# Optimization experiments

Hardware: AMD Instinct MI355X
Metric: run time of the kernel (lower is better)

Reference implementation:

```python
import jax, jax.numpy as jnp
import numpy as np

P = 920   # spatial positions per frame (hard-coded in source)
FRAMES = 5
H = 8     # num_heads
C = 256   # dim


def setup_inputs() -> dict:
    key = jax.random.key(0)
    ks = jax.random.split(key, 6)
    B = 4
    s = 0.02
    return {
        "x": jax.random.normal(ks[0], (P, B * FRAMES, C), dtype=jnp.float32),
        "W_qkv": jax.random.normal(ks[1], (3 * C, C), dtype=jnp.float32) * s,
        "W_pq": jax.random.normal(ks[2], (C, C), dtype=jnp.float32) * s,
        "W_pkv": jax.random.normal(ks[3], (2 * C, C), dtype=jnp.float32) * s,
        "W_proj": jax.random.normal(ks[4], (C, C), dtype=jnp.float32) * s,
        "b_proj": jnp.zeros((C,), dtype=jnp.float32),
    }


def reference(x, W_qkv, W_pq, W_pkv, W_proj, b_proj):
    d = C // H
    scale = d ** -0.5
    N = FRAMES * P

    # (P, B*F, C) -> (B*F, P, C) -> (B, F*P, C)
    xb = jnp.transpose(x, (1, 0, 2)).reshape(-1, N, C)
    B = xb.shape[0]

    # Stage 1: space attention (note: heads are NOT split here, per original code)
    qkv = xb @ W_qkv.T                      # (B, N, 3C)
    q_, k_, v_ = jnp.split(qkv, 3, axis=-1)
    q_dot_k = jnp.einsum('bqc,bnc->bqn', q_, k_)        # (B, N, N)
    q_dot_k = q_dot_k.reshape(B, N, FRAMES, P)          # b q f n
    space_attn = jax.nn.softmax(scale * q_dot_k, axis=-1)
    v_f = v_.reshape(B, FRAMES, P, C)                   # b f n d
    x1 = jnp.einsum('bqfn,bfnd->bqfd', space_attn, v_f)  # (B, N, F, C)

    # Diagonal extraction: each spatial position attends to its own frame
    xg = x1.reshape(B, FRAMES, P, FRAMES, C)            # b g n f d
    x_diag = jnp.diagonal(xg, axis1=1, axis2=3)         # (B, P, C, F)
    x_diag = jnp.transpose(x_diag, (0, 3, 1, 2)).reshape(B, N, C)  # b (f n) d

    # Stage 2: trajectory attention over frames, with heads
    q2 = x_diag @ W_pq.T                                # (B, N, C)
    kv2 = x1 @ W_pkv.T                                  # (B, N, F, 2C)
    k2, v2 = jnp.split(kv2, 2, axis=-1)
    q2 = q2.reshape(B, N, H, d).transpose(0, 2, 1, 3) * scale      # b h s d
    k2 = k2.reshape(B, N, FRAMES, H, d).transpose(0, 3, 1, 2, 4)   # b h s f d
    v2 = v2.reshape(B, N, FRAMES, H, d).transpose(0, 3, 1, 2, 4)
    attn = jax.nn.softmax(jnp.einsum('bhsd,bhsfd->bhsf', q2, k2), axis=-1)
    x2 = jnp.einsum('bhsf,bhsfd->bhsd', attn, v2)       # (B, H, N, d)
    x2 = x2.transpose(0, 2, 1, 3).reshape(B, N, C)

    out = x2 @ W_proj.T + b_proj                        # (B, N, C)
    out = out.reshape(B, FRAMES, P, C).reshape(B * FRAMES, P, C)
    out = jnp.transpose(out, (1, 0, 2))                 # (P, B*F, C)
    return out, attn
```

## Files before the change

### kernel.cpp

```cpp
#include <hip/hip_runtime.h>
#include <stdint.h>

#define PP 920
#define FF 5
#define BBATCH 4
#define CC 256
#define NN 4600
#define HH 8
#define MROWS 18400
#define M2ROWS 92000
#define SCALE 0.17677669529663687f


typedef short bf16x8 __attribute__((ext_vector_type(8)));
typedef float f32x4 __attribute__((ext_vector_type(4)));
typedef uint32_t u32;

#define MFMA16 __builtin_amdgcn_mfma_f32_16x16x32_bf16

__device__ __forceinline__ float b2f(unsigned short s){
  u32 u = ((u32)s) << 16; float f; __builtin_memcpy(&f, &u, 4); return f;
}
__device__ __forceinline__ unsigned short f2b(float f){
  u32 u; __builtin_memcpy(&u, &f, 4);
  u = (u + 0x7FFFu + ((u >> 16) & 1u)) >> 16;
  return (unsigned short)u;
}


__global__ void k19_cast(const float* __restrict__ in, short* __restrict__ out, int n){
  int i = blockIdx.x*256 + threadIdx.x;
  if (i < n) out[i] = (short)f2b(in[i]);
}

__global__ void k19_make_xb(const float* __restrict__ x, short* __restrict__ xb){
  int i = blockIdx.x*256 + threadIdx.x;
  long e0 = (long)i*4;
  if (e0 >= (long)MROWS*CC) return;
  int row = (int)(e0 >> 8); int c = (int)(e0 & 255);
  int b = row / NN; int s = row - b*NN; int f = s / PP; int p = s - f*PP;
  const float4 v = *(const float4*)(x + ((size_t)(p*(BBATCH*FF) + b*FF + f))*CC + c);
  unsigned short o[4];
  o[0]=f2b(v.x); o[1]=f2b(v.y); o[2]=f2b(v.z); o[3]=f2b(v.w);
  *(ushort4*)(xb + e0) = *(ushort4*)o;
}

__global__ void k19_zero(short* p, int n){
  int i = blockIdx.x*256 + threadIdx.x;
  if (i < n) p[i] = 0;
}

template<int MODE>
__launch_bounds__(256)
__global__ void k19_gemm(const short* __restrict__ A, const short* __restrict__ Bw,
                         short* __restrict__ Cout, float* __restrict__ FCout,
                         const float* __restrict__ bias,
                         int M, int lda, int ldc, float alpha)
{
  __shared__ short As[128][40];
  __shared__ short Bs[128][40];
  const int tid = threadIdx.x;
  const int m0 = blockIdx.x*128, n0 = blockIdx.y*128;
  const int w = tid >> 6, l = tid & 63;
  const int wm = (w >> 1)*64, wn = (w & 1)*64;
  const int lr = l & 15, lg = l >> 4;

  f32x4 acc[4][4] = {};

  for (int k0 = 0; k0 < 256; k0 += 32){
    #pragma unroll
    for (int i = 0; i < 2; i++){
      int v = tid + 256*i;
      int ar = v >> 2, as = (v & 3)*8;
      int grow = m0 + ar; if (grow >= M) grow = M - 1;
      *(uint4*)(&As[ar][as]) = *(const uint4*)(A + (size_t)grow*lda + k0 + as);
      *(uint4*)(&Bs[ar][as]) = *(const uint4*)(Bw + (size_t)(n0 + ar)*256 + k0 + as);
    }
    __syncthreads();
    bf16x8 af[4], bfr[4];
    #pragma unroll
    for (int i = 0; i < 4; i++) af[i]  = *(const bf16x8*)(&As[wm + i*16 + lr][lg*8]);
    #pragma unroll
    for (int j = 0; j < 4; j++) bfr[j] = *(const bf16x8*)(&Bs[wn + j*16 + lr][lg*8]);
    #pragma unroll
    for (int i = 0; i < 4; i++)
      #pragma unroll
      for (int j = 0; j < 4; j++)
        acc[i][j] = MFMA16(af[i], bfr[j], acc[i][j], 0, 0, 0);
    __syncthreads();
  }

  #pragma unroll
  for (int i = 0; i < 4; i++){
    #pragma unroll
    for (int r = 0; r < 4; r++){
      int m = m0 + wm + i*16 + lg*4 + r;
      if (m >= M) continue;
      #pragma unroll
      for (int j = 0; j < 4; j++){
        int n = n0 + wn + j*16 + lr;
        float v = acc[i][j][r]*alpha;
        if (MODE == 1){
          v += bias[n];
          int b = m / NN, s = m - b*NN; int f = s / PP, p = s - f*PP;
          FCout[(size_t)(p*(BBATCH*FF) + b*FF + f)*CC + n] = v;
        } else {
          Cout[(size_t)m*ldc + n] = (short)f2b(v);
        }
      }
    }
  }
}

__launch_bounds__(256)
__global__ void k19_vt(const short* __restrict__ qkv, short* __restrict__ vt){
  __shared__ short t[64][80];
  const int p0 = blockIdx.x*64;
  const int c0 = blockIdx.y*64;
  const int bf = blockIdx.z;
  const int b = bf / FF, f = bf - b*FF;
  const int tid = threadIdx.x;
  #pragma unroll
  for (int i = 0; i < 2; i++){
    int v = tid + 256*i;
    int pr = v >> 3, sg = (v & 7)*8;
    uint4 val = make_uint4(0,0,0,0);
    int p = p0 + pr;
    if (p < PP)
      val = *(const uint4*)(qkv + ((size_t)(b*NN + f*PP + p))*768 + 512 + c0 + sg);
    *(uint4*)(&t[pr][sg]) = val;
  }
  __syncthreads();
  #pragma unroll
  for (int i = 0; i < 2; i++){
    int v = tid + 256*i;
    int cr = v & 63, pg = v >> 6;
    int pbase = p0 + pg*8;
    if (pbase < 928){
      unsigned short o[8];
      #pragma unroll
      for (int jj = 0; jj < 8; jj++) o[jj] = (unsigned short)t[pg*8 + jj][cr];
      *(uint4*)(vt + ((size_t)(bf*CC + c0 + cr))*928 + pbase) = *(uint4*)o;
    }
  }
}

__launch_bounds__(256)
__global__ void k19_flash(const short* __restrict__ qkv, const short* __restrict__ vt,
                          short* __restrict__ x1, short* __restrict__ xd)
{
  __shared__ short Ks[32][264];
  __shared__ short Vs[256][40];
  __shared__ short Ps[64][40];

  const int qt = blockIdx.x, f = blockIdx.y, b = blockIdx.z;
  const int tid = threadIdx.x, w = tid >> 6, l = tid & 63;
  const int lr = l & 15, lg = l >> 4;
  const int qbase = qt*64;

  bf16x8 qf[8];
  {
    int qrow = qbase + w*16 + lr; if (qrow > NN - 1) qrow = NN - 1;
    const short* qp = qkv + (size_t)(b*NN + qrow)*768;
    #pragma unroll
    for (int kc = 0; kc < 8; kc++) qf[kc] = *(const bf16x8*)(qp + kc*32 + lg*8);
  }

  f32x4 o[16] = {};
  float den[4] = {0.f, 0.f, 0.f, 0.f};

  const size_t krow0 = (size_t)(b*NN + f*PP)*768 + 256;
  const short* vtp = vt + (size_t)((b*FF + f)*CC)*928;

  for (int ch = 0; ch < 29; ch++){
    const int key0 = ch*32;
    #pragma unroll
    for (int i = 0; i < 4; i++){
      int v = tid + 256*i;
      int kr = v >> 5, ks = (v & 31)*8;
      *(uint4*)(&Ks[kr][ks]) = *(const uint4*)(qkv + krow0 + (size_t)(key0 + kr)*768 + ks);
    }
    {
      const short* vp = vtp + (size_t)tid*928 + key0;
      #pragma unroll
      for (int i = 0; i < 4; i++)
        *(uint4*)(&Vs[tid][i*8]) = *(const uint4*)(vp + i*8);
    }
    __syncthreads();

    f32x4 s0 = {}, s1 = {};
    #pragma unroll
    for (int kc = 0; kc < 8; kc++){
      bf16x8 k0v = *(const bf16x8*)(&Ks[lr][kc*32 + lg*8]);
      bf16x8 k1v = *(const bf16x8*)(&Ks[16 + lr][kc*32 + lg*8]);
      s0 = MFMA16(qf[kc], k0v, s0, 0, 0, 0);
      s1 = MFMA16(qf[kc], k1v, s1, 0, 0, 0);
    }

    #pragma unroll
    for (int r = 0; r < 4; r++){
      float v0 = s0[r]*SCALE, v1 = s1[r]*SCALE;
      if (key0 + lr      >= PP) v0 = -1e30f;
      if (key0 + 16 + lr >= PP) v1 = -1e30f;
      float p0 = __expf(v0);
      float p1 = __expf(v1);
      den[r] += p0 + p1;
      int qlocal = w*16 + lg*4 + r;
      Ps[qlocal][lr]      = (short)f2b(p0);
      Ps[qlocal][16 + lr] = (short)f2b(p1);
    }

    bf16x8 pa = *(const bf16x8*)(&Ps[w*16 + lr][lg*8]);
    #pragma unroll
    for (int ct = 0; ct < 16; ct++){
      bf16x8 vb = *(const bf16x8*)(&Vs[ct*16 + lr][lg*8]);
      o[ct] = MFMA16(pa, vb, o[ct], 0, 0, 0);
    }
    __syncthreads();
  }

  #pragma unroll
  for (int r = 0; r < 4; r++){
    float dsum = den[r];
    #pragma unroll
    for (int off = 8; off >= 1; off >>= 1) dsum += __shfl_xor(dsum, off);
    float inv = 1.f/dsum;
    int srow = qbase + w*16 + lg*4 + r;
    if (srow >= NN) continue;
    bool dg = (srow/PP == f);
    size_t x1base = ((size_t)(b*NN + srow)*FF + f)*CC;
    size_t xdbase = (size_t)(b*NN + srow)*CC;
    #pragma unroll
    for (int ct = 0; ct < 16; ct++){
      short val = (short)f2b(o[ct][r]*inv);
      x1[x1base + ct*16 + lr] = val;
      if (dg) xd[xdbase + ct*16 + lr] = val;
    }
  }
}

__launch_bounds__(256)
__global__ void k19_attn2(const short* __restrict__ q2b, const short* __restrict__ k2v2,
                          float* __restrict__ attnp, short* __restrict__ x2)
{
  int idx = blockIdx.x*256 + threadIdx.x;
  if (idx >= MROWS*HH) return;
  const int h = idx & 7; const int row = idx >> 3;

  float qv[32];
  {
    const short* qp = q2b + (size_t)row*CC + h*32;
    #pragma unroll
    for (int s4 = 0; s4 < 4; s4++){
      uint4 u = *(const uint4*)(qp + s4*8);
      const unsigned short* sp = (const unsigned short*)&u;
      #pragma unroll
      for (int j = 0; j < 8; j++) qv[s4*8 + j] = b2f(sp[j]);
    }
  }

  float lgt[FF];
  #pragma unroll
  for (int f = 0; f < FF; f++){
    const short* kp = k2v2 + ((size_t)row*FF + f)*512 + h*32;
    float a = 0.f;
    #pragma unroll
    for (int s4 = 0; s4 < 4; s4++){
      uint4 u = *(const uint4*)(kp + s4*8);
      const unsigned short* sp = (const unsigned short*)&u;
      #pragma unroll
      for (int j = 0; j < 8; j++) a += qv[s4*8 + j]*b2f(sp[j]);
    }
    lgt[f] = a;
  }

  float mx = lgt[0];
  #pragma unroll
  for (int f = 1; f < FF; f++) mx = fmaxf(mx, lgt[f]);
  float pr[FF], ps = 0.f;
  #pragma unroll
  for (int f = 0; f < FF; f++){ pr[f] = __expf(lgt[f] - mx); ps += pr[f]; }
  float inv = 1.f/ps;

  const int b = row / NN; const int s = row - b*NN;
  size_t ab = (((size_t)(b*HH + h))*NN + s)*FF;
  #pragma unroll
  for (int f = 0; f < FF; f++) attnp[ab + f] = pr[f]*inv;

  float xa[32] = {};
  #pragma unroll
  for (int f = 0; f < FF; f++){
    const short* vp = k2v2 + ((size_t)row*FF + f)*512 + 256 + h*32;
    float wgt = pr[f]*inv;
    #pragma unroll
    for (int s4 = 0; s4 < 4; s4++){
      uint4 u = *(const uint4*)(vp + s4*8);
      const unsigned short* sp = (const unsigned short*)&u;
      #pragma unroll
      for (int j = 0; j < 8; j++) xa[s4*8 + j] += wgt*b2f(sp[j]);
    }
  }
  #pragma unroll
  for (int s4 = 0; s4 < 4; s4++){
    unsigned short o[8];
    #pragma unroll
    for (int j = 0; j < 8; j++) o[j] = f2b(xa[s4*8 + j]);
    *(uint4*)(x2 + (size_t)row*CC + h*32 + s4*8) = *(uint4*)o;
  }
}

extern "C" void kernel_launch(void* const* d_in, const int* in_sizes, int n_in,
                              void* d_out, int out_size, void* d_ws, size_t ws_size,
                              hipStream_t stream)
{
  int ix=-1, iwqkv=-1, iwpq=-1, iwpkv=-1, iwproj=-1, ib=-1;
  for (int i = 0; i < n_in; i++){
    switch (in_sizes[i]){
      case 4710400: ix = i; break;
      case 196608:  iwqkv = i; break;
      case 131072:  iwpkv = i; break;
      case 256:     ib = i; break;
      case 65536:   if (iwpq < 0) iwpq = i; else iwproj = i; break;
      default: break;
    }
  }
  if (ix < 0 || iwqkv < 0 || iwpq < 0 || iwpkv < 0 || iwproj < 0 || ib < 0){
    ix=0; iwqkv=1; iwpq=2; iwpkv=3; iwproj=4; ib=5;
  }
  const float* x     = (const float*)d_in[ix];
  const float* Wqkv  = (const float*)d_in[iwqkv];
  const float* Wpq   = (const float*)d_in[iwpq];
  const float* Wpkv  = (const float*)d_in[iwpkv];
  const float* Wproj = (const float*)d_in[iwproj];
  const float* bproj = (const float*)d_in[ib];

  char* ws = (char*)d_ws;
  if (ws_size < 208269312ULL) return;

  short* wq    = (short*)(ws + 0);
  short* wpq   = (short*)(ws + 393216);
  short* wpkv  = (short*)(ws + 524288);
  short* wprj  = (short*)(ws + 786432);
  short* xb    = (short*)(ws + 917504);
  short* qkv   = (short*)(ws + 10338304);
  short* vt    = (short*)(ws + 38612992);
  short* x1    = (short*)(ws + 48115712);
  short* xd    = (short*)(ws + 95219712);
  short* k2v2  = (short*)(ws + 104640512);
  short* q2b   = (short*)(ws + 198848512);
  short* x2    = xb;

  float* outp  = (float*)d_out;
  float* attnp = outp + 4710400;

  k19_cast<<<dim3(768), dim3(256), 0, stream>>>(Wqkv,  wq,   196608);
  k19_cast<<<dim3(256), dim3(256), 0, stream>>>(Wpq,   wpq,  65536);
  k19_cast<<<dim3(512), dim3(256), 0, stream>>>(Wpkv,  wpkv, 131072);
  k19_cast<<<dim3(256), dim3(256), 0, stream>>>(Wproj, wprj, 65536);
  k19_make_xb<<<dim3(4600), dim3(256), 0, stream>>>(x, xb);
  k19_zero<<<dim3(24), dim3(256), 0, stream>>>(qkv + (size_t)MROWS*768, 6144);

  k19_gemm<0><<<dim3(144, 6), dim3(256), 0, stream>>>(xb, wq, qkv, nullptr, nullptr, MROWS, 256, 768, 1.0f);
  k19_vt<<<dim3(15, 4, 20), dim3(256), 0, stream>>>(qkv, vt);
  k19_flash<<<dim3(72, 5, 4), dim3(256), 0, stream>>>(qkv, vt, x1, xd);
  k19_gemm<0><<<dim3(719, 4), dim3(256), 0, stream>>>(x1, wpkv, k2v2, nullptr, nullptr, M2ROWS, 256, 512, 1.0f);
  k19_gemm<0><<<dim3(144, 2), dim3(256), 0, stream>>>(xd, wpq, q2b, nullptr, nullptr, MROWS, 256, 256, SCALE);
  k19_attn2<<<dim3(575), dim3(256), 0, stream>>>(q2b, k2v2, attnp, x2);
  k19_gemm<1><<<dim3(144, 2), dim3(256), 0, stream>>>(x2, wprj, nullptr, outp, bproj, MROWS, 256, 256, 1.0f);
}
```

Baseline: 322.5 us.

## Process 128 query rows per flash block to reuse K/V tiles

Each flash-attention block now handles two 64-row query tiles instead of one. Every K and V chunk loaded into shared memory therefore feeds twice the MFMA work, and the grid is halved. The softmax switches from exp to exp2 with a pre-folded log2(e) scale, and key masking is limited to the final chunk. The trade-off is roughly double the accumulator registers (two sets of 16 f32x4 outputs), which may reduce occupancy or cause spilling, and fewer blocks to spread across the CUs.

After: 350.9 us. 1.09x slower.

```diff
diff --git a/kernel.cpp b/kernel.cpp
--- a/kernel.cpp
+++ b/kernel.cpp
@@ -10,6 +10,7 @@
 #define MROWS 18400
 #define M2ROWS 92000
 #define SCALE 0.17677669529663687f
+#define SCALE_L2E (0.17677669529663687f * 1.4426950408889634f)
 
 
 typedef short bf16x8 __attribute__((ext_vector_type(8)));
@@ -28,12 +29,12 @@
 }
 
 
-__global__ void k19_cast(const float* __restrict__ in, short* __restrict__ out, int n){
+__global__ void k20_cast(const float* __restrict__ in, short* __restrict__ out, int n){
   int i = blockIdx.x*256 + threadIdx.x;
   if (i < n) out[i] = (short)f2b(in[i]);
 }
 
-__global__ void k19_make_xb(const float* __restrict__ x, short* __restrict__ xb){
+__global__ void k20_make_xb(const float* __restrict__ x, short* __restrict__ xb){
   int i = blockIdx.x*256 + threadIdx.x;
   long e0 = (long)i*4;
   if (e0 >= (long)MROWS*CC) return;
@@ -45,14 +46,14 @@
   *(ushort4*)(xb + e0) = *(ushort4*)o;
 }
 
-__global__ void k19_zero(short* p, int n){
+__global__ void k20_zero(short* p, int n){
   int i = blockIdx.x*256 + threadIdx.x;
   if (i < n) p[i] = 0;
 }
 
 template<int MODE>
 __launch_bounds__(256)
-__global__ void k19_gemm(const short* __restrict__ A, const short* __restrict__ Bw,
+__global__ void k20_gemm(const short* __restrict__ A, const short* __restrict__ Bw,
                          short* __restrict__ Cout, float* __restrict__ FCout,
                          const float* __restrict__ bias,
                          int M, int lda, int ldc, float alpha)
@@ -113,7 +114,7 @@
 }
 
 __launch_bounds__(256)
-__global__ void k19_vt(const short* __restrict__ qkv, short* __restrict__ vt){
+__global__ void k20_vt(const short* __restrict__ qkv, short* __restrict__ vt){
   __shared__ short t[64][80];
   const int p0 = blockIdx.x*64;
   const int c0 = blockIdx.y*64;
@@ -146,28 +147,33 @@
 }
 
 __launch_bounds__(256)
-__global__ void k19_flash(const short* __restrict__ qkv, const short* __restrict__ vt,
+__global__ void k20_flash(const short* __restrict__ qkv, const short* __restrict__ vt,
                           short* __restrict__ x1, short* __restrict__ xd)
 {
   __shared__ short Ks[32][264];
   __shared__ short Vs[256][40];
-  __shared__ short Ps[64][40];
+  __shared__ short Ps[128][40];
 
   const int qt = blockIdx.x, f = blockIdx.y, b = blockIdx.z;
   const int tid = threadIdx.x, w = tid >> 6, l = tid & 63;
   const int lr = l & 15, lg = l >> 4;
-  const int qbase = qt*64;
-
-  bf16x8 qf[8];
+  const int qbase = qt*128;
+
+  bf16x8 qf0[8], qf1[8];
   {
-    int qrow = qbase + w*16 + lr; if (qrow > NN - 1) qrow = NN - 1;
-    const short* qp = qkv + (size_t)(b*NN + qrow)*768;
-    #pragma unroll
-    for (int kc = 0; kc < 8; kc++) qf[kc] = *(const bf16x8*)(qp + kc*32 + lg*8);
-  }
-
-  f32x4 o[16] = {};
-  float den[4] = {0.f, 0.f, 0.f, 0.f};
+    int qr0 = qbase + w*16 + lr;      if (qr0 > NN - 1) qr0 = NN - 1;
+    int qr1 = qbase + 64 + w*16 + lr; if (qr1 > NN - 1) qr1 = NN - 1;
+    const short* qp0 = qkv + (size_t)(b*NN + qr0)*768;
+    const short* qp1 = qkv + (size_t)(b*NN + qr1)*768;
+    #pragma unroll
+    for (int kc = 0; kc < 8; kc++){
+      qf0[kc] = *(const bf16x8*)(qp0 + kc*32 + lg*8);
+      qf1[kc] = *(const bf16x8*)(qp1 + kc*32 + lg*8);
+    }
+  }
+
+  f32x4 o0[16] = {}, o1[16] = {};
+  float den0[4] = {}, den1[4] = {};
 
   const size_t krow0 = (size_t)(b*NN + f*PP)*768 + 256;
   const short* vtp = vt + (size_t)((b*FF + f)*CC)*928;
@@ -188,59 +194,74 @@
     }
     __syncthreads();
 
-    f32x4 s0 = {}, s1 = {};
+    f32x4 s00 = {}, s01 = {}, s10 = {}, s11 = {};
     #pragma unroll
     for (int kc = 0; kc < 8; kc++){
       bf16x8 k0v = *(const bf16x8*)(&Ks[lr][kc*32 + lg*8]);
       bf16x8 k1v = *(const bf16x8*)(&Ks[16 + lr][kc*32 + lg*8]);
-      s0 = MFMA16(qf[kc], k0v, s0, 0, 0, 0);
-      s1 = MFMA16(qf[kc], k1v, s1, 0, 0, 0);
-    }
-
+      s00 = MFMA16(qf0[kc], k0v, s00, 0, 0, 0);
+      s01 = MFMA16(qf0[kc], k1v, s01, 0, 0, 0);
+      s10 = MFMA16(qf1[kc], k0v, s10, 0, 0, 0);
+      s11 = MFMA16(qf1[kc], k1v, s11, 0, 0, 0);
+    }
+
+    const bool masked = (ch == 28);
     #pragma unroll
     for (int r = 0; r < 4; r++){
-      float v0 = s0[r]*SCALE, v1 = s1[r]*SCALE;
-      if (key0 + lr      >= PP) v0 = -1e30f;
-      if (key0 + 16 + lr >= PP) v1 = -1e30f;
-      float p0 = __expf(v0);
-      float p1 = __expf(v1);
-      den[r] += p0 + p1;
-      int qlocal = w*16 + lg*4 + r;
-      Ps[qlocal][lr]      = (short)f2b(p0);
-      Ps[qlocal][16 + lr] = (short)f2b(p1);
-    }
-
-    bf16x8 pa = *(const bf16x8*)(&Ps[w*16 + lr][lg*8]);
+      float v00 = s00[r]*SCALE_L2E, v01 = s01[r]*SCALE_L2E;
+      float v10 = s10[r]*SCALE_L2E, v11 = s11[r]*SCALE_L2E;
+      if (masked){
+        if (key0 + lr      >= PP){ v00 = -1e30f; v10 = -1e30f; }
+        if (key0 + 16 + lr >= PP){ v01 = -1e30f; v11 = -1e30f; }
+      }
+      float p00 = exp2f(v00), p01 = exp2f(v01);
+      float p10 = exp2f(v10), p11 = exp2f(v11);
+      den0[r] += p00 + p01;
+      den1[r] += p10 + p11;
+      int q0 = w*16 + lg*4 + r;
+      Ps[q0][lr]           = (short)f2b(p00);
+      Ps[q0][16 + lr]      = (short)f2b(p01);
+      Ps[64 + q0][lr]      = (short)f2b(p10);
+      Ps[64 + q0][16 + lr] = (short)f2b(p11);
+    }
+
+    bf16x8 pa0 = *(const bf16x8*)(&Ps[w*16 + lr][lg*8]);
+    bf16x8 pa1 = *(const bf16x8*)(&Ps[64 + w*16 + lr][lg*8]);
     #pragma unroll
     for (int ct = 0; ct < 16; ct++){
       bf16x8 vb = *(const bf16x8*)(&Vs[ct*16 + lr][lg*8]);
-      o[ct] = MFMA16(pa, vb, o[ct], 0, 0, 0);
+      o0[ct] = MFMA16(pa0, vb, o0[ct], 0, 0, 0);
+      o1[ct] = MFMA16(pa1, vb, o1[ct], 0, 0, 0);
     }
     __syncthreads();
   }
 
   #pragma unroll
-  for (int r = 0; r < 4; r++){
-    float dsum = den[r];
-    #pragma unroll
-    for (int off = 8; off >= 1; off >>= 1) dsum += __shfl_xor(dsum, off);
-    float inv = 1.f/dsum;
-    int srow = qbase + w*16 + lg*4 + r;
-    if (srow >= NN) continue;
-    bool dg = (srow/PP == f);
-    size_t x1base = ((size_t)(b*NN + srow)*FF + f)*CC;
-    size_t xdbase = (size_t)(b*NN + srow)*CC;
-    #pragma unroll
-    for (int ct = 0; ct < 16; ct++){
-      short val = (short)f2b(o[ct][r]*inv);
-      x1[x1base + ct*16 + lr] = val;
-      if (dg) xd[xdbase + ct*16 + lr] = val;
+  for (int t = 0; t < 2; t++){
+    #pragma unroll
+    for (int r = 0; r < 4; r++){
+      float dsum = t ? den1[r] : den0[r];
+      #pragma unroll
+      for (int off = 8; off >= 1; off >>= 1) dsum += __shfl_xor(dsum, off);
+      float inv = 1.f/dsum;
+      int srow = qbase + t*64 + w*16 + lg*4 + r;
+      if (srow >= NN) continue;
+      bool dg = (srow/PP == f);
+      size_t x1base = ((size_t)(b*NN + srow)*FF + f)*CC;
+      size_t xdbase = (size_t)(b*NN + srow)*CC;
+      #pragma unroll
+      for (int ct = 0; ct < 16; ct++){
+        float ov = t ? o1[ct][r] : o0[ct][r];
+        short val = (short)f2b(ov*inv);
+        x1[x1base + ct*16 + lr] = val;
+        if (dg) xd[xdbase + ct*16 + lr] = val;
+      }
     }
   }
 }
 
 __launch_bounds__(256)
-__global__ void k19_attn2(const short* __restrict__ q2b, const short* __restrict__ k2v2,
+__global__ void k20_attn2(const short* __restrict__ q2b, const short* __restrict__ k2v2,
                           float* __restrict__ attnp, short* __restrict__ x2)
 {
   int idx = blockIdx.x*256 + threadIdx.x;
@@ -353,18 +374,18 @@
   float* outp  = (float*)d_out;
   float* attnp = outp + 4710400;
 
-  k19_cast<<<dim3(768), dim3(256), 0, stream>>>(Wqkv,  wq,   196608);
-  k19_cast<<<dim3(256), dim3(256), 0, stream>>>(Wpq,   wpq,  65536);
-  k19_cast<<<dim3(512), dim3(256), 0, stream>>>(Wpkv,  wpkv, 131072);
-  k19_cast<<<dim3(256), dim3(256), 0, stream>>>(Wproj, wprj, 65536);
-  k19_make_xb<<<dim3(4600), dim3(256), 0, stream>>>(x, xb);
-  k19_zero<<<dim3(24), dim3(256), 0, stream>>>(qkv + (size_t)MROWS*768, 6144);
-
-  k19_gemm<0><<<dim3(144, 6), dim3(256), 0, stream>>>(xb, wq, qkv, nullptr, nullptr, MROWS, 256, 768, 1.0f);
-  k19_vt<<<dim3(15, 4, 20), dim3(256), 0, stream>>>(qkv, vt);
-  k19_flash<<<dim3(72, 5, 4), dim3(256), 0, stream>>>(qkv, vt, x1, xd);
-  k19_gemm<0><<<dim3(719, 4), dim3(256), 0, stream>>>(x1, wpkv, k2v2, nullptr, nullptr, M2ROWS, 256, 512, 1.0f);
-  k19_gemm<0><<<dim3(144, 2), dim3(256), 0, stream>>>(xd, wpq, q2b, nullptr, nullptr, MROWS, 256, 256, SCALE);
-  k19_attn2<<<dim3(575), dim3(256), 0, stream>>>(q2b, k2v2, attnp, x2);
-  k19_gemm<1><<<dim3(144, 2), dim3(256), 0, stream>>>(x2, wprj, nullptr, outp, bproj, MROWS, 256, 256, 1.0f);
-}
+  k20_cast<<<dim3(768), dim3(256), 0, stream>>>(Wqkv,  wq,   196608);
+  k20_cast<<<dim3(256), dim3(256), 0, stream>>>(Wpq,   wpq,  65536);
+  k20_cast<<<dim3(512), dim3(256), 0, stream>>>(Wpkv,  wpkv, 131072);
+  k20_cast<<<dim3(256), dim3(256), 0, stream>>>(Wproj, wprj, 65536);
+  k20_make_xb<<<dim3(4600), dim3(256), 0, stream>>>(x, xb);
+  k20_zero<<<dim3(24), dim3(256), 0, stream>>>(qkv + (size_t)MROWS*768, 6144);
+
+  k20_gemm<0><<<dim3(144, 6), dim3(256), 0, stream>>>(xb, wq, qkv, nullptr, nullptr, MROWS, 256, 768, 1.0f);
+  k20_vt<<<dim3(15, 4, 20), dim3(256), 0, stream>>>(qkv, vt);
+  k20_flash<<<dim3(36, 5, 4), dim3(256), 0, stream>>>(qkv, vt, x1, xd);
+  k20_gemm<0><<<dim3(719, 4), dim3(256), 0, stream>>>(x1, wpkv, k2v2, nullptr, nullptr, M2ROWS, 256, 512, 1.0f);
+  k20_gemm<0><<<dim3(144, 2), dim3(256), 0, stream>>>(xd, wpq, q2b, nullptr, nullptr, MROWS, 256, 256, SCALE);
+  k20_attn2<<<dim3(575), dim3(256), 0, stream>>>(q2b, k2v2, attnp, x2);
+  k20_gemm<1><<<dim3(144, 2), dim3(256), 0, stream>>>(x2, wprj, nullptr, outp, bproj, MROWS, 256, 256, 1.0f);
+}
```
